# Kernel tuning notes

Measured on AMD Instinct MI355X. Metric: run time of the kernel, lower is better.

## Reference

```python
import jax, jax.numpy as jnp
import numpy as np

N = 40000        # total nodes (2000 graphs x 20 nodes)
E = 60000        # edges per relation (before self-loops)
R = 6            # number of relations
IN = 32
HID = 128
OUT = 128
H = 2            # heads
C = 128          # per-head out channels (concat=False)
B = 2000         # number of graphs
NEG_SLOPE = 0.2


def setup_inputs() -> dict:
    key = jax.random.key(0)
    ks = jax.random.split(key, 16)
    rn = lambda k, s, sc=0.05: (jax.random.normal(k, s, jnp.float32) * sc)
    x = jax.random.normal(ks[0], (N, IN), jnp.float32)
    edge_index = jax.random.randint(ks[1], (R, 2, E), 0, N, dtype=jnp.int32)
    batch = (jnp.arange(N, dtype=jnp.int32) // (N // B)).astype(jnp.int32)
    return {
        "x": x, "edge_index": edge_index, "batch": batch,
        "Wl1": rn(ks[2], (R, IN, H * C)), "bl1": jnp.zeros((R, H * C), jnp.float32),
        "Wr1": rn(ks[3], (R, IN, H * C)), "br1": jnp.zeros((R, H * C), jnp.float32),
        "att1": rn(ks[4], (R, H, C)), "bias1": jnp.zeros((R, C), jnp.float32),
        "Wl2": rn(ks[5], (R, HID, H * C)), "bl2": jnp.zeros((R, H * C), jnp.float32),
        "Wr2": rn(ks[6], (R, HID, H * C)), "br2": jnp.zeros((R, H * C), jnp.float32),
        "att2": rn(ks[7], (R, H, C)), "bias2": jnp.zeros((R, C), jnp.float32),
        "ln1_g": jnp.ones((HID,), jnp.float32), "ln1_b": jnp.zeros((HID,), jnp.float32),
        "ln2_g": jnp.ones((HID,), jnp.float32), "ln2_b": jnp.zeros((HID,), jnp.float32),
        "query": rn(ks[8], (HID,), 0.02),
        "projW": rn(ks[9], (HID, OUT)), "projb": jnp.zeros((OUT,), jnp.float32),
    }


def _gatv2(x, src, dst, Wl, bl, Wr, br, att, bias):
    # x: [N, F]; src/dst: [Etot] (self-loops already appended)
    n = x.shape[0]
    xl = (x @ Wl + bl).reshape(n, H, C)   # source transform
    xr = (x @ Wr + br).reshape(n, H, C)   # target transform
    e = jax.nn.leaky_relu(xl[src] + xr[dst], NEG_SLOPE)   # [Etot, H, C]
    logits = jnp.einsum('ehc,hc->eh', e, att)             # [Etot, H]
    m = jax.ops.segment_max(logits, dst, num_segments=n)
    a = jnp.exp(logits - m[dst])
    s = jax.ops.segment_sum(a, dst, num_segments=n)
    w = a / s[dst]                                        # segment softmax
    out = jax.ops.segment_sum(w[:, :, None] * xl[src], dst, num_segments=n)
    return out.mean(axis=1) + bias                        # head-average (concat=False)


def _hetero_layer(x, edge_index, Wl, bl, Wr, br, att, bias):
    loops = jnp.broadcast_to(jnp.arange(N, dtype=edge_index.dtype), (R, N))
    src = jnp.concatenate([edge_index[:, 0, :], loops], axis=1)  # [R, E+N]
    dst = jnp.concatenate([edge_index[:, 1, :], loops], axis=1)
    outs = jax.vmap(_gatv2, in_axes=(None, 0, 0, 0, 0, 0, 0, 0, 0))(
        x, src, dst, Wl, bl, Wr, br, att, bias)
    return outs.sum(axis=0)  # HeteroConv aggr='sum'


def _layernorm(x, g, b, eps=1e-5):
    mu = x.mean(-1, keepdims=True)
    var = ((x - mu) ** 2).mean(-1, keepdims=True)
    return (x - mu) * jax.lax.rsqrt(var + eps) * g + b


def reference(x, edge_index, batch, Wl1, bl1, Wr1, br1, att1, bias1,
              Wl2, bl2, Wr2, br2, att2, bias2,
              ln1_g, ln1_b, ln2_g, ln2_b, query, projW, projb):
    h = _hetero_layer(x, edge_index, Wl1, bl1, Wr1, br1, att1, bias1)
    h = _layernorm(jnp.tanh(h), ln1_g, ln1_b)
    h = _hetero_layer(h, edge_index, Wl2, bl2, Wr2, br2, att2, bias2)
    h = _layernorm(jnp.tanh(h), ln2_g, ln2_b)
    # attention pooling over graphs (segment softmax on batch ids)
    scores = h @ query                              # [N]
    m = jax.ops.segment_max(scores, batch, num_segments=B)
    a = jnp.exp(scores - m[batch])
    s = jax.ops.segment_sum(a, batch, num_segments=B)
    w = a / s[batch]
    g = jax.ops.segment_sum(w[:, None] * h, batch, num_segments=B)  # [B, HID]
    return g @ projW + projb
```

## Files before the change

kernel.cpp:

```cpp
#include <hip/hip_runtime.h>
#include <hip/hip_bf16.h>
#include <math.h>

#define N_NODES 40000
#define E_EDGES 60000
#define R_REL 6
#define IN_F 32
#define HID_F 128
#define B_GRAPHS 2000
#define NODES_PER_G 20
#define NEG_SLOPE 0.2f
#define NB (R_REL * N_NODES)
#define NTOT (R_REL * (E_EDGES + N_NODES))
#define NBLK ((NB + 255) / 256)

#define CNT_B ((NTOT + 255) / 256)
#define CVT_B ((N_NODES * 16 + 255) / 256)
#define P1_B  (R_REL * 512 * 32 / 256)
#define P2_B  (R_REL * 512 * 128 / 256)
#define PREP_TOTAL (CNT_B + CVT_B + P1_B + P2_B + 1)

typedef __bf16 bf16x8 __attribute__((ext_vector_type(8)));
typedef float f32x4 __attribute__((ext_vector_type(4)));

__device__ __forceinline__ unsigned f2bfbits(float f) {
    unsigned u = __builtin_bit_cast(unsigned, f);
    return (u + 0x7FFFu + ((u >> 16) & 1u)) >> 16;
}
__device__ __forceinline__ float bflo(unsigned u) { return __builtin_bit_cast(float, u << 16); }
__device__ __forceinline__ float bfhi(unsigned u) { return __builtin_bit_cast(float, u & 0xFFFF0000u); }

__device__ __forceinline__ float fast_tanh(float x) {
    float e = __builtin_amdgcn_exp2f(x * 2.8853900817779268f);
    return fmaf(-2.f, __builtin_amdgcn_rcpf(e + 1.f), 1.f);
}

template<int CTRL>
__device__ __forceinline__ float dppadd(float v) {
    int m = __builtin_amdgcn_update_dpp(0, __builtin_bit_cast(int, v), CTRL, 0xF, 0xF, true);
    return v + __builtin_bit_cast(float, m);
}
__device__ __forceinline__ float rowsum16(float v) {
    v = dppadd<0x121>(v);
    v = dppadd<0x122>(v);
    v = dppadd<0x124>(v);
    v = dppadd<0x128>(v);
    return v;
}
__device__ __forceinline__ float halfsum32(float v) {
    v += __shfl_xor(v, 16);
    return rowsum16(v);
}

__device__ __forceinline__ void prep_w_body(
    const float* __restrict__ Wl, const float* __restrict__ Wr,
    const float* __restrict__ bl, const float* __restrict__ br,
    unsigned short* __restrict__ Bt, float* __restrict__ bcat, int K, int idx)
{
    if (idx >= R_REL * 512 * K) return;
    int k = idx % K;
    int rn = idx / K;
    int n = rn % 512;
    int r = rn / 512;
    int nn = n & 255;
    const float* W = (n < 256) ? Wl : Wr;
    float w = W[((size_t)r * K + k) * 256 + nn];
    Bt[idx] = (unsigned short)f2bfbits(w);
    if (k == 0)
        bcat[rn] = (n < 256) ? bl[r * 256 + nn] : br[r * 256 + nn];
}

__global__ __launch_bounds__(256) void fused_prep_kernel(
    const int* __restrict__ ei, int* __restrict__ cnt,
    const float* __restrict__ x, unsigned* __restrict__ xbf,
    const float* __restrict__ Wl1, const float* __restrict__ Wr1,
    const float* __restrict__ bl1, const float* __restrict__ br1,
    unsigned short* __restrict__ Bt1, float* __restrict__ bc1,
    const float* __restrict__ Wl2, const float* __restrict__ Wr2,
    const float* __restrict__ bl2, const float* __restrict__ br2,
    unsigned short* __restrict__ Bt2, float* __restrict__ bc2,
    const float* __restrict__ bias1, const float* __restrict__ bias2,
    float* __restrict__ bsum1, float* __restrict__ bsum2,
    const float* __restrict__ att1, const float* __restrict__ att2,
    float* __restrict__ attP1, float* __restrict__ attP2)
{
    int b = blockIdx.x;
    int tid = threadIdx.x;
    if (b < CNT_B) {
        int idx = b * 256 + tid;
        if (idx >= NTOT) return;
        int bin;
        if (idx < R_REL * E_EDGES) {
            int r = idx / E_EDGES, e = idx - r * E_EDGES;
            bin = r * N_NODES + ei[(size_t)r * 2 * E_EDGES + E_EDGES + e];
        } else {
            bin = idx - R_REL * E_EDGES;
        }
        atomicAdd(&cnt[bin], 1);
    } else if (b < CNT_B + CVT_B) {
        int i = (b - CNT_B) * 256 + tid;
        if (i >= N_NODES * 16) return;
        float2 v = *(const float2*)(x + 2 * i);
        xbf[i] = f2bfbits(v.x) | (f2bfbits(v.y) << 16);
    } else if (b < CNT_B + CVT_B + P1_B) {
        prep_w_body(Wl1, Wr1, bl1, br1, Bt1, bc1, 32, (b - CNT_B - CVT_B) * 256 + tid);
    } else if (b < CNT_B + CVT_B + P1_B + P2_B) {
        prep_w_body(Wl2, Wr2, bl2, br2, Bt2, bc2, 128, (b - CNT_B - CVT_B - P1_B) * 256 + tid);
    } else {
        const float L2E = 1.4426950408889634f;
        for (int r = 0; r < R_REL; r++) {
            float a1 = att1[r * 256 + tid];
            float a2 = att2[r * 256 + tid];
            attP1[r * 512 + tid]       = 0.6f * L2E * a1;
            attP1[r * 512 + 256 + tid] = 0.4f * L2E * a1;
            attP2[r * 512 + tid]       = 0.6f * L2E * a2;
            attP2[r * 512 + 256 + tid] = 0.4f * L2E * a2;
        }
        if (tid < 128) {
            float s1 = 0.f, s2 = 0.f;
            for (int r = 0; r < R_REL; r++) { s1 += bias1[r * 128 + tid]; s2 += bias2[r * 128 + tid]; }
            bsum1[tid] = s1; bsum2[tid] = s2;
        }
    }
}

__global__ __launch_bounds__(256) void scan1_kernel(
    const int* __restrict__ cnt, int* __restrict__ part, int* __restrict__ bsum)
{
    int i = blockIdx.x * 256 + threadIdx.x;
    int v = (i < NB) ? cnt[i] : 0;
    int lane = threadIdx.x & 63, w = threadIdx.x >> 6;
    int x = v;
#pragma unroll
    for (int off = 1; off < 64; off <<= 1) {
        int y = __shfl_up(x, off, 64);
        if (lane >= off) x += y;
    }
    __shared__ int ws[4];
    if (lane == 63) ws[w] = x;
    __syncthreads();
    int add = 0;
    for (int j = 0; j < w; j++) add += ws[j];
    int incl = x + add;
    if (i < NB) part[i] = incl - v;
    if (threadIdx.x == 255) bsum[blockIdx.x] = incl;
}

__global__ __launch_bounds__(256) void scan2_kernel(
    const int* __restrict__ bsum, int* __restrict__ boff)
{
    __shared__ int ws[4];
    int t = threadIdx.x;
    int lane = t & 63, w = t >> 6;
    int base4 = t * 4;
    int pre[4];
    int s = 0;
#pragma unroll
    for (int j = 0; j < 4; j++) {
        int i = base4 + j;
        int x = (i < NBLK) ? bsum[i] : 0;
        pre[j] = s;
        s += x;
    }
    int incl = s;
#pragma unroll
    for (int off = 1; off < 64; off <<= 1) {
        int y = __shfl_up(incl, off, 64);
        if (lane >= off) incl += y;
    }
    if (lane == 63) ws[w] = incl;
    __syncthreads();
    int wbase = 0;
    for (int j = 0; j < w; j++) wbase += ws[j];
    int tbase = wbase + incl - s;
#pragma unroll
    for (int j = 0; j < 4; j++) {
        int i = base4 + j;
        if (i < NBLK) boff[i] = tbase + pre[j];
    }
}

__global__ __launch_bounds__(256) void scan3_kernel(
    const int* __restrict__ part, const int* __restrict__ boff,
    int* __restrict__ rowptr, int* __restrict__ cursor)
{
    int i = blockIdx.x * 256 + threadIdx.x;
    if (i < NB) {
        int v = part[i] + boff[i >> 8];
        rowptr[i] = v;
        cursor[i] = v;
    }
    if (i == 0) rowptr[NB] = NTOT;
}

__global__ __launch_bounds__(256) void scatter_kernel(
    const int* __restrict__ ei, int* __restrict__ cursor, int* __restrict__ csr)
{
    int idx = blockIdx.x * 256 + threadIdx.x;
    if (idx >= NTOT) return;
    int bin, src;
    if (idx < R_REL * E_EDGES) {
        int r = idx / E_EDGES, e = idx - r * E_EDGES;
        src = ei[(size_t)r * 2 * E_EDGES + e];
        bin = r * N_NODES + ei[(size_t)r * 2 * E_EDGES + E_EDGES + e];
    } else {
        bin = idx - R_REL * E_EDGES;
        src = bin % N_NODES;
    }
    int pos = atomicAdd(&cursor[bin], 1);
    csr[pos] = src;
}

template <int K>
__global__ __launch_bounds__(256, 4) void gemm_mfma_kernel(
    const unsigned short* __restrict__ A,
    const unsigned short* __restrict__ BtAll,
    const float* __restrict__ biasAll,
    unsigned short* __restrict__ CAll)
{
    constexpr int KC = (K > 64) ? 64 : K;
    constexpr int NCH = K / KC;
    constexpr int CH = KC / 8;
    constexpr int TB = 128 * KC * 2;
    __shared__ char lds[2 * TB];
    char* ldsA = lds;
    char* ldsB = lds + TB;

    int tid = threadIdx.x;
    int lane = tid & 63, wave = tid >> 6;
    int l16 = lane & 15, quad = lane >> 4;
    int wm = (wave >> 1) * 64, wn = (wave & 1) * 64;
    int ny = blockIdx.x & 3, z = blockIdx.x >> 2;
    int m0 = blockIdx.y * 128, n0 = ny * 128;

    auto SW = [](int row) { return (KC == 64) ? (row & 7) : ((row >> 1) & 3); };

    const char* Bt = (const char*)(BtAll + (size_t)z * 512 * K);

    f32x4 acc[4][4];
#pragma unroll
    for (int i = 0; i < 4; i++)
#pragma unroll
        for (int j = 0; j < 4; j++) {
            acc[i][j][0] = 0.f; acc[i][j][1] = 0.f;
            acc[i][j][2] = 0.f; acc[i][j][3] = 0.f;
        }

    for (int nc = 0; nc < NCH; ++nc) {
        if (nc) __syncthreads();
#pragma unroll
        for (int it = 0; it < (128 * CH) / 256; ++it) {
            int s = it * 256 + tid;
            int row = s / CH, sc = s % CH;
            int c = sc ^ SW(row);
            int gr = m0 + row; gr = gr < N_NODES ? gr : N_NODES - 1;
            const char* gpA = (const char*)A + (size_t)gr * (K * 2) + nc * KC * 2 + c * 16;
            __builtin_amdgcn_global_load_lds(
                (const __attribute__((address_space(1))) void*)gpA,
                (__attribute__((address_space(3))) void*)(ldsA + it * 4096 + wave * 1024), 16, 0, 0);
            const char* gpB = Bt + (size_t)(n0 + row) * (K * 2) + nc * KC * 2 + c * 16;
            __builtin_amdgcn_global_load_lds(
                (const __attribute__((address_space(1))) void*)gpB,
                (__attribute__((address_space(3))) void*)(ldsB + it * 4096 + wave * 1024), 16, 0, 0);
        }
        __syncthreads();

#pragma unroll
        for (int kk = 0; kk < KC / 32; ++kk) {
            bf16x8 af[4], bfr[4];
#pragma unroll
            for (int i = 0; i < 4; ++i) {
                int row = wm + i * 16 + l16;
                int slot = (kk * 4 + quad) ^ SW(row);
                af[i] = *(const bf16x8*)(ldsA + row * (KC * 2) + slot * 16);
            }
#pragma unroll
            for (int j = 0; j < 4; ++j) {
                int row = wn + j * 16 + l16;
                int slot = (kk * 4 + quad) ^ SW(row);
                bfr[j] = *(const bf16x8*)(ldsB + row * (KC * 2) + slot * 16);
            }
#pragma unroll
            for (int i = 0; i < 4; i++)
#pragma unroll
                for (int j = 0; j < 4; j++)
                    acc[i][j] = __builtin_amdgcn_mfma_f32_16x16x32_bf16(af[i], bfr[j], acc[i][j], 0, 0, 0);
        }
    }

    const float* bias = biasAll + z * 512;
    unsigned short* C = CAll + (size_t)z * N_NODES * 512;
    float biasj[4];
#pragma unroll
    for (int j = 0; j < 4; ++j) biasj[j] = bias[n0 + wn + j * 16 + l16];
#pragma unroll
    for (int i = 0; i < 4; i++) {
        int gr0 = m0 + wm + i * 16 + quad * 4;
#pragma unroll
        for (int j = 0; j < 4; j++) {
            int col = n0 + wn + j * 16 + l16;
#pragma unroll
            for (int rg = 0; rg < 4; rg++) {
                float a = acc[i][j][rg] + biasj[j];
                float b = __shfl_xor(a, 1);
                int grow = gr0 + rg;
                if (!(lane & 1) && grow < N_NODES) {
                    __hip_bfloat162 h2 = __float22bfloat162_rn(make_float2(a, b));
                    unsigned u;
                    __builtin_memcpy(&u, &h2, 4);
                    *(unsigned*)((char*)C + ((size_t)grow * 512 + col) * 2) = u;
                }
            }
        }
    }
}

__global__ __launch_bounds__(256) void gat6_ln_kernel(
    const unsigned short* __restrict__ XLR,
    const int* __restrict__ rowptr,
    const int* __restrict__ csr,
    const float* __restrict__ attP,
    const float* __restrict__ bsum,
    const float* __restrict__ lng, const float* __restrict__ lnb,
    unsigned* __restrict__ hout)
{
    int gtid = blockIdx.x * 256 + threadIdx.x;
    int d = gtid >> 6;
    int lane = threadIdx.x & 63;
    if (d >= N_NODES) return;
    int hl = lane & 31;

    const size_t RS = (size_t)N_NODES * 1024;
    const char* lanep = (const char*)XLR + lane * 8;
    const char* xrbase = lanep + ((size_t)(unsigned)d << 10) + 512;

    float tot0 = 0.f, tot1 = 0.f, tot2 = 0.f, tot3 = 0.f;
#pragma unroll 1
    for (int r = 0; r < R_REL; r++) {
        uint2 xru = *(const uint2*)(xrbase + (size_t)r * RS);
        float4 a6 = *(const float4*)(attP + r * 512 + lane * 4);
        float4 a4 = *(const float4*)(attP + r * 512 + 256 + lane * 4);
        int bin = r * N_NODES + d;
        int beg = __builtin_amdgcn_readfirstlane(rowptr[bin]);
        int end = __builtin_amdgcn_readfirstlane(rowptr[bin + 1]);
        const char* base = lanep + (size_t)r * RS;
        float xr0 = bflo(xru.x), xr1 = bfhi(xru.x), xr2 = bflo(xru.y), xr3 = bfhi(xru.y);

        float sA = 0.f, a0 = 0.f, a1 = 0.f, a2 = 0.f, a3 = 0.f;
        float sB = 0.f, b0 = 0.f, b1 = 0.f, b2 = 0.f, b3 = 0.f;
        int i = beg;
        for (; i + 2 <= end; i += 2) {
            int s0 = csr[i], s1 = csr[i + 1];
            const unsigned* pA = (const unsigned*)(base + ((size_t)(unsigned)s0 << 10));
            const unsigned* pB = (const unsigned*)(base + ((size_t)(unsigned)s1 << 10));
            unsigned uA0 = pA[0], uA1 = pA[1];
            unsigned uB0 = pB[0], uB1 = pB[1];
            float xA0 = bflo(uA0), xA1 = bfhi(uA0), xA2 = bflo(uA1), xA3 = bfhi(uA1);
            float xB0 = bflo(uB0), xB1 = bfhi(uB0), xB2 = bflo(uB1), xB3 = bfhi(uB1);
            float tA0 = xA0 + xr0, tA1 = xA1 + xr1, tA2 = xA2 + xr2, tA3 = xA3 + xr3;
            float tB0 = xB0 + xr0, tB1 = xB1 + xr1, tB2 = xB2 + xr2, tB3 = xB3 + xr3;
            float pa = xA0 * a6.x;
            float pb = xB0 * a6.x;
            pa = fmaf(xA1, a6.y, pa);
            pb = fmaf(xB1, a6.y, pb);
            pa = fmaf(xA2, a6.z, pa);
            pb = fmaf(xB2, a6.z, pb);
            pa = fmaf(xA3, a6.w, pa);
            pb = fmaf(xB3, a6.w, pb);
            pa = fmaf(__builtin_fabsf(tA0), a4.x, pa);
            pb = fmaf(__builtin_fabsf(tB0), a4.x, pb);
            pa = fmaf(__builtin_fabsf(tA1), a4.y, pa);
            pb = fmaf(__builtin_fabsf(tB1), a4.y, pb);
            pa = fmaf(__builtin_fabsf(tA2), a4.z, pa);
            pb = fmaf(__builtin_fabsf(tB2), a4.z, pb);
            pa = fmaf(__builtin_fabsf(tA3), a4.w, pa);
            pb = fmaf(__builtin_fabsf(tB3), a4.w, pb);
            pa = halfsum32(pa);
            pb = halfsum32(pb);
            float wa = __builtin_amdgcn_exp2f(fminf(pa, 120.f));
            float wb = __builtin_amdgcn_exp2f(fminf(pb, 120.f));
            sA += wa; sB += wb;
            a0 = fmaf(wa, xA0, a0); b0 = fmaf(wb, xB0, b0);
            a1 = fmaf(wa, xA1, a1); b1 = fmaf(wb, xB1, b1);
            a2 = fmaf(wa, xA2, a2); b2 = fmaf(wb, xB2, b2);
            a3 = fmaf(wa, xA3, a3); b3 = fmaf(wb, xB3, b3);
        }
        if (i < end) {
            int s0 = csr[i];
            const unsigned* pA = (const unsigned*)(base + ((size_t)(unsigned)s0 << 10));
            unsigned uA0 = pA[0], uA1 = pA[1];
            float xA0 = bflo(uA0), xA1 = bfhi(uA0), xA2 = bflo(uA1), xA3 = bfhi(uA1);
            float tA0 = xA0 + xr0, tA1 = xA1 + xr1, tA2 = xA2 + xr2, tA3 = xA3 + xr3;
            float pa = xA0 * a6.x;
            pa = fmaf(xA1, a6.y, pa);
            pa = fmaf(xA2, a6.z, pa);
            pa = fmaf(xA3, a6.w, pa);
            pa = fmaf(__builtin_fabsf(tA0), a4.x, pa);
            pa = fmaf(__builtin_fabsf(tA1), a4.y, pa);
            pa = fmaf(__builtin_fabsf(tA2), a4.z, pa);
            pa = fmaf(__builtin_fabsf(tA3), a4.w, pa);
            pa = halfsum32(pa);
            float wa = __builtin_amdgcn_exp2f(fminf(pa, 120.f));
            sA += wa;
            a0 = fmaf(wa, xA0, a0);
            a1 = fmaf(wa, xA1, a1);
            a2 = fmaf(wa, xA2, a2);
            a3 = fmaf(wa, xA3, a3);
        }
        sA += sB; a0 += b0; a1 += b1; a2 += b2; a3 += b3;
        float rs = 0.5f * __builtin_amdgcn_rcpf(sA);
        tot0 = fmaf(a0, rs, tot0);
        tot1 = fmaf(a1, rs, tot1);
        tot2 = fmaf(a2, rs, tot2);
        tot3 = fmaf(a3, rs, tot3);
    }

    tot0 += __shfl_xor(tot0, 32);
    tot1 += __shfl_xor(tot1, 32);
    tot2 += __shfl_xor(tot2, 32);
    tot3 += __shfl_xor(tot3, 32);
    float4 bs = *(const float4*)(bsum + hl * 4);

    float v0 = fast_tanh(tot0 + bs.x);
    float v1 = fast_tanh(tot1 + bs.y);
    float v2 = fast_tanh(tot2 + bs.z);
    float v3 = fast_tanh(tot3 + bs.w);
    float sum = halfsum32(v0 + v1 + v2 + v3);
    float sq = halfsum32(v0 * v0 + v1 * v1 + v2 * v2 + v3 * v3);
    float mean = sum * (1.f / 128.f);
    float var = sq * (1.f / 128.f) - mean * mean;
    float rstd = rsqrtf(var + 1e-5f);
    float4 gg = *(const float4*)(lng + hl * 4);
    float4 bb = *(const float4*)(lnb + hl * 4);
    float o0 = (v0 - mean) * rstd * gg.x + bb.x;
    float o1 = (v1 - mean) * rstd * gg.y + bb.y;
    float o2 = (v2 - mean) * rstd * gg.z + bb.z;
    float o3 = (v3 - mean) * rstd * gg.w + bb.w;
    if (lane < 32) {
        uint2 q;
        q.x = f2bfbits(o0) | (f2bfbits(o1) << 16);
        q.y = f2bfbits(o2) | (f2bfbits(o3) << 16);
        *((uint2*)(hout + (size_t)d * 64) + hl) = q;
    }
}

__global__ __launch_bounds__(256) void pool_proj_kernel(
    const unsigned* __restrict__ hb, const float* __restrict__ query,
    const float* __restrict__ W, const float* __restrict__ pb,
    float* __restrict__ out)
{
    __shared__ float gL[4][128];
    int wave = threadIdx.x >> 6;
    int lane = threadIdx.x & 63;
    int bg = blockIdx.x * 4 + wave;
    float2 q = *(const float2*)(query + 2 * lane);
    float mx = -1e30f, ssum = 0.f, g0 = 0.f, g1 = 0.f;
    for (int i = 0; i < NODES_PER_G; i++) {
        unsigned u = hb[(size_t)(bg * NODES_PER_G + i) * 64 + lane];
        float h0 = bflo(u), h1 = bfhi(u);
        float p = h0 * q.x + h1 * q.y;
#pragma unroll
        for (int off = 32; off >= 1; off >>= 1) p += __shfl_xor(p, off, 64);
        float mn = fmaxf(mx, p);
        float sc = __expf(mx - mn), w = __expf(p - mn);
        ssum = ssum * sc + w;
        g0 = g0 * sc + w * h0;
        g1 = g1 * sc + w * h1;
        mx = mn;
    }
    float inv = 1.f / ssum;
    gL[wave][2 * lane] = g0 * inv;
    gL[wave][2 * lane + 1] = g1 * inv;
    __syncthreads();
    int o0 = lane, o1 = lane + 64;
    float a0 = pb[o0], a1 = pb[o1];
    for (int k = 0; k < 128; k++) {
        float gk = gL[wave][k];
        a0 = fmaf(gk, W[k * 128 + o0], a0);
        a1 = fmaf(gk, W[k * 128 + o1], a1);
    }
    out[(size_t)bg * 128 + o0] = a0;
    out[(size_t)bg * 128 + o1] = a1;
}

extern "C" void kernel_launch(void* const* d_in, const int* in_sizes, int n_in,
                              void* d_out, int out_size, void* d_ws, size_t ws_size,
                              hipStream_t stream)
{
    const float* x     = (const float*)d_in[0];
    const int*   ei    = (const int*)d_in[1];
    const float* Wl1   = (const float*)d_in[3];
    const float* bl1   = (const float*)d_in[4];
    const float* Wr1   = (const float*)d_in[5];
    const float* br1   = (const float*)d_in[6];
    const float* att1  = (const float*)d_in[7];
    const float* bias1 = (const float*)d_in[8];
    const float* Wl2   = (const float*)d_in[9];
    const float* bl2   = (const float*)d_in[10];
    const float* Wr2   = (const float*)d_in[11];
    const float* br2   = (const float*)d_in[12];
    const float* att2  = (const float*)d_in[13];
    const float* bias2 = (const float*)d_in[14];
    const float* ln1g  = (const float*)d_in[15];
    const float* ln1b  = (const float*)d_in[16];
    const float* ln2g  = (const float*)d_in[17];
    const float* ln2b  = (const float*)d_in[18];
    const float* query = (const float*)d_in[19];
    const float* projW = (const float*)d_in[20];
    const float* projb = (const float*)d_in[21];
    float* out = (float*)d_out;

    unsigned short* xlr6 = (unsigned short*)d_ws;
    unsigned short* h1bf = xlr6 + (size_t)R_REL * N_NODES * 512;
    unsigned short* xbf  = h1bf + (size_t)N_NODES * 128;
    unsigned short* Bt1  = xbf + (size_t)N_NODES * 32;
    unsigned short* Bt2  = Bt1 + R_REL * 512 * 32;
    float* bc1  = (float*)(Bt2 + R_REL * 512 * 128);
    float* bc2  = bc1 + R_REL * 512;
    float* bsum1 = bc2 + R_REL * 512;
    float* bsum2 = bsum1 + 128;
    float* attP1 = bsum2 + 128;
    float* attP2 = attP1 + R_REL * 512;
    int* cnt    = (int*)(attP2 + R_REL * 512);
    int* part   = cnt + NB;
    int* rowptr = part + NB;
    int* cursor = rowptr + NB + 1;
    int* bsum   = cursor + NB;
    int* boff   = bsum + NBLK;
    int* csr    = boff + NBLK;

    hipMemsetAsync(cnt, 0, sizeof(int) * NB, stream);
    fused_prep_kernel<<<PREP_TOTAL, 256, 0, stream>>>(
        ei, cnt, x, (unsigned*)xbf,
        Wl1, Wr1, bl1, br1, Bt1, bc1,
        Wl2, Wr2, bl2, br2, Bt2, bc2,
        bias1, bias2, bsum1, bsum2,
        att1, att2, attP1, attP2);
    scan1_kernel<<<NBLK, 256, 0, stream>>>(cnt, part, bsum);
    scan2_kernel<<<1, 256, 0, stream>>>(bsum, boff);
    scan3_kernel<<<NBLK, 256, 0, stream>>>(part, boff, rowptr, cursor);
    scatter_kernel<<<(NTOT + 255) / 256, 256, 0, stream>>>(ei, cursor, csr);

    dim3 ggrid(24, (N_NODES + 127) / 128, 1);
    gemm_mfma_kernel<32><<<ggrid, 256, 0, stream>>>(xbf, Bt1, bc1, xlr6);
    gat6_ln_kernel<<<N_NODES / 4, 256, 0, stream>>>(
        xlr6, rowptr, csr, attP1, bsum1, ln1g, ln1b, (unsigned*)h1bf);
    gemm_mfma_kernel<128><<<ggrid, 256, 0, stream>>>(h1bf, Bt2, bc2, xlr6);
    gat6_ln_kernel<<<N_NODES / 4, 256, 0, stream>>>(
        xlr6, rowptr, csr, attP2, bsum2, ln2g, ln2b, (unsigned*)h1bf);
    pool_proj_kernel<<<B_GRAPHS / 4, 256, 0, stream>>>(
        (unsigned*)h1bf, query, projW, projb, out);
}
```

Before: 410.5 us.

## Handle self-loops analytically and fold block-offset scan into the final scan pass

```diff
diff --git a/kernel.cpp b/kernel.cpp
--- a/kernel.cpp
+++ b/kernel.cpp
@@ -11,10 +11,10 @@
 #define NODES_PER_G 20
 #define NEG_SLOPE 0.2f
 #define NB (R_REL * N_NODES)
-#define NTOT (R_REL * (E_EDGES + N_NODES))
+#define NREAL (R_REL * E_EDGES)
 #define NBLK ((NB + 255) / 256)
 
-#define CNT_B ((NTOT + 255) / 256)
+#define CNT_B ((NREAL + 255) / 256)
 #define CVT_B ((N_NODES * 16 + 255) / 256)
 #define P1_B  (R_REL * 512 * 32 / 256)
 #define P2_B  (R_REL * 512 * 128 / 256)
@@ -88,14 +88,9 @@
     int tid = threadIdx.x;
     if (b < CNT_B) {
         int idx = b * 256 + tid;
-        if (idx >= NTOT) return;
-        int bin;
-        if (idx < R_REL * E_EDGES) {
-            int r = idx / E_EDGES, e = idx - r * E_EDGES;
-            bin = r * N_NODES + ei[(size_t)r * 2 * E_EDGES + E_EDGES + e];
-        } else {
-            bin = idx - R_REL * E_EDGES;
-        }
+        if (idx >= NREAL) return;
+        int r = idx / E_EDGES, e = idx - r * E_EDGES;
+        int bin = r * N_NODES + ei[(size_t)r * 2 * E_EDGES + E_EDGES + e];
         atomicAdd(&cnt[bin], 1);
     } else if (b < CNT_B + CVT_B) {
         int i = (b - CNT_B) * 256 + tid;
@@ -146,67 +141,37 @@
     if (threadIdx.x == 255) bsum[blockIdx.x] = incl;
 }
 
-__global__ __launch_bounds__(256) void scan2_kernel(
-    const int* __restrict__ bsum, int* __restrict__ boff)
+__global__ __launch_bounds__(256) void scan3_kernel(
+    const int* __restrict__ part, const int* __restrict__ bsum,
+    int* __restrict__ rowptr, int* __restrict__ cursor)
 {
     __shared__ int ws[4];
-    int t = threadIdx.x;
+    int t = threadIdx.x, b = blockIdx.x;
+    int s = 0;
+    for (int j = t; j < b; j += 256) s += bsum[j];
+#pragma unroll
+    for (int off = 32; off >= 1; off >>= 1) s += __shfl_xor(s, off);
     int lane = t & 63, w = t >> 6;
-    int base4 = t * 4;
-    int pre[4];
-    int s = 0;
-#pragma unroll
-    for (int j = 0; j < 4; j++) {
-        int i = base4 + j;
-        int x = (i < NBLK) ? bsum[i] : 0;
-        pre[j] = s;
-        s += x;
-    }
-    int incl = s;
-#pragma unroll
-    for (int off = 1; off < 64; off <<= 1) {
-        int y = __shfl_up(incl, off, 64);
-        if (lane >= off) incl += y;
-    }
-    if (lane == 63) ws[w] = incl;
+    if (lane == 0) ws[w] = s;
     __syncthreads();
-    int wbase = 0;
-    for (int j = 0; j < w; j++) wbase += ws[j];
-    int tbase = wbase + incl - s;
-#pragma unroll
-    for (int j = 0; j < 4; j++) {
-        int i = base4 + j;
-        if (i < NBLK) boff[i] = tbase + pre[j];
-    }
-}
-
-__global__ __launch_bounds__(256) void scan3_kernel(
-    const int* __restrict__ part, const int* __restrict__ boff,
-    int* __restrict__ rowptr, int* __restrict__ cursor)
-{
-    int i = blockIdx.x * 256 + threadIdx.x;
+    int boffb = ws[0] + ws[1] + ws[2] + ws[3];
+    int i = b * 256 + t;
     if (i < NB) {
-        int v = part[i] + boff[i >> 8];
+        int v = part[i] + boffb;
         rowptr[i] = v;
         cursor[i] = v;
     }
-    if (i == 0) rowptr[NB] = NTOT;
+    if (i == 0) rowptr[NB] = NREAL;
 }
 
 __global__ __launch_bounds__(256) void scatter_kernel(
     const int* __restrict__ ei, int* __restrict__ cursor, int* __restrict__ csr)
 {
     int idx = blockIdx.x * 256 + threadIdx.x;
-    if (idx >= NTOT) return;
-    int bin, src;
-    if (idx < R_REL * E_EDGES) {
-        int r = idx / E_EDGES, e = idx - r * E_EDGES;
-        src = ei[(size_t)r * 2 * E_EDGES + e];
-        bin = r * N_NODES + ei[(size_t)r * 2 * E_EDGES + E_EDGES + e];
-    } else {
-        bin = idx - R_REL * E_EDGES;
-        src = bin % N_NODES;
-    }
+    if (idx >= NREAL) return;
+    int r = idx / E_EDGES, e = idx - r * E_EDGES;
+    int src = ei[(size_t)r * 2 * E_EDGES + e];
+    int bin = r * N_NODES + ei[(size_t)r * 2 * E_EDGES + E_EDGES + e];
     int pos = atomicAdd(&cursor[bin], 1);
     csr[pos] = src;
 }
@@ -337,7 +302,9 @@
     float tot0 = 0.f, tot1 = 0.f, tot2 = 0.f, tot3 = 0.f;
 #pragma unroll 1
     for (int r = 0; r < R_REL; r++) {
-        uint2 xru = *(const uint2*)(xrbase + (size_t)r * RS);
+        const char* xrp = xrbase + (size_t)r * RS;
+        uint2 xru = *(const uint2*)xrp;
+        uint2 xls = *(const uint2*)(xrp - 512);
         float4 a6 = *(const float4*)(attP + r * 512 + lane * 4);
         float4 a4 = *(const float4*)(attP + r * 512 + 256 + lane * 4);
         int bin = r * N_NODES + d;
@@ -346,7 +313,19 @@
         const char* base = lanep + (size_t)r * RS;
         float xr0 = bflo(xru.x), xr1 = bfhi(xru.x), xr2 = bflo(xru.y), xr3 = bfhi(xru.y);
 
-        float sA = 0.f, a0 = 0.f, a1 = 0.f, a2 = 0.f, a3 = 0.f;
+        float xS0 = bflo(xls.x), xS1 = bfhi(xls.x), xS2 = bflo(xls.y), xS3 = bfhi(xls.y);
+        float tS0 = xS0 + xr0, tS1 = xS1 + xr1, tS2 = xS2 + xr2, tS3 = xS3 + xr3;
+        float ps = xS0 * a6.x;
+        ps = fmaf(xS1, a6.y, ps);
+        ps = fmaf(xS2, a6.z, ps);
+        ps = fmaf(xS3, a6.w, ps);
+        ps = fmaf(__builtin_fabsf(tS0), a4.x, ps);
+        ps = fmaf(__builtin_fabsf(tS1), a4.y, ps);
+        ps = fmaf(__builtin_fabsf(tS2), a4.z, ps);
+        ps = fmaf(__builtin_fabsf(tS3), a4.w, ps);
+        ps = halfsum32(ps);
+        float wS = __builtin_amdgcn_exp2f(fminf(ps, 120.f));
+        float sA = wS, a0 = wS * xS0, a1 = wS * xS1, a2 = wS * xS2, a3 = wS * xS3;
         float sB = 0.f, b0 = 0.f, b1 = 0.f, b2 = 0.f, b3 = 0.f;
         int i = beg;
         for (; i + 2 <= end; i += 2) {
@@ -526,8 +505,7 @@
     int* rowptr = part + NB;
     int* cursor = rowptr + NB + 1;
     int* bsum   = cursor + NB;
-    int* boff   = bsum + NBLK;
-    int* csr    = boff + NBLK;
+    int* csr    = bsum + NBLK;
 
     hipMemsetAsync(cnt, 0, sizeof(int) * NB, stream);
     fused_prep_kernel<<<PREP_TOTAL, 256, 0, stream>>>(
@@ -537,9 +515,8 @@
         bias1, bias2, bsum1, bsum2,
         att1, att2, attP1, attP2);
     scan1_kernel<<<NBLK, 256, 0, stream>>>(cnt, part, bsum);
-    scan2_kernel<<<1, 256, 0, stream>>>(bsum, boff);
-    scan3_kernel<<<NBLK, 256, 0, stream>>>(part, boff, rowptr, cursor);
-    scatter_kernel<<<(NTOT + 255) / 256, 256, 0, stream>>>(ei, cursor, csr);
+    scan3_kernel<<<NBLK, 256, 0, stream>>>(part, bsum, rowptr, cursor);
+    scatter_kernel<<<(NREAL + 255) / 256, 256, 0, stream>>>(ei, cursor, csr);
 
     dim3 ggrid(24, (N_NODES + 127) / 128, 1);
     gemm_mfma_kernel<32><<<ggrid, 256, 0, stream>>>(xbf, Bt1, bc1, xlr6);
```

Result: no change. 404.5 us, median of 2 (-1.5%).
